# Optimization experiments

Hardware: AMD Instinct MI355X
Metric: run time of the kernel (lower is better)

Reference implementation:

```python
import jax, jax.numpy as jnp
import numpy as np

B, C, H, W = 4, 256, 64, 64
C8 = C // 8


def setup_inputs() -> dict:
    key = jax.random.key(0)
    ks = jax.random.split(key, 7)
    return {
        "x": jax.random.normal(ks[0], (B, C, H, W), dtype=jnp.float32),
        "Wq": jax.random.normal(ks[1], (C8, C), dtype=jnp.float32) * 0.05,
        "bq": jax.random.normal(ks[2], (C8,), dtype=jnp.float32) * 0.05,
        "Wk": jax.random.normal(ks[3], (C8, C), dtype=jnp.float32) * 0.05,
        "bk": jax.random.normal(ks[4], (C8,), dtype=jnp.float32) * 0.05,
        "Wv": jax.random.normal(ks[5], (C, C), dtype=jnp.float32) * 0.05,
        "bv": jax.random.normal(ks[6], (C,), dtype=jnp.float32) * 0.05,
        "gamma": jnp.zeros((1,), dtype=jnp.float32),
    }


def reference(x, Wq, bq, Wk, bk, Wv, bv, gamma):
    b, c, h, w = x.shape
    n = h * w
    xf = x.reshape(b, c, n)  # [B, C, N]
    # 1x1 convs == per-pixel linear maps over channels
    q = jnp.einsum('oc,bcn->bon', Wq, xf) + bq[None, :, None]  # [B, C/8, N]
    k = jnp.einsum('oc,bcn->bon', Wk, xf) + bk[None, :, None]  # [B, C/8, N]
    v = jnp.einsum('oc,bcn->bon', Wv, xf) + bv[None, :, None]  # [B, C, N]
    # s[b,i,j] = q_i . k_j ; torch softmax over dim=-2 (the i axis)
    s = jnp.einsum('bci,bcj->bij', q, k)  # [B, N, N]
    attn_T = jax.nn.softmax(s, axis=-2)
    # o[b,c,j] = sum_i v[b,c,i] * attn_T[b,i,j]
    o = jnp.einsum('bci,bij->bcj', v, attn_T)  # [B, C, N]
    return x + gamma[0] * o.reshape(b, c, h, w)
```

## Files before the change

kernel.cpp:

```cpp
#include <hip/hip_runtime.h>
#include <hip/hip_bf16.h>


typedef float  f32x16 __attribute__((ext_vector_type(16)));
typedef float  f32x4  __attribute__((ext_vector_type(4)));
typedef short  s16x8  __attribute__((ext_vector_type(8)));
typedef unsigned int u32;
typedef unsigned int u32x4 __attribute__((ext_vector_type(4)));

__device__ __forceinline__ s16x8 ld16(const ushort* p) {
  return *reinterpret_cast<const s16x8*>(p);
}
__device__ __forceinline__ ushort f2bf(float f) {
  return (ushort)((__float_as_uint(f) + 0x8000u) >> 16);
}
__device__ __forceinline__ u32 cvt_pk_bf16(float lo, float hi) {
  u32 r;
  asm("v_cvt_pk_bf16_f32 %0, %1, %2" : "=v"(r) : "v"(lo), "v"(hi));
  return r;
}

__global__ void wf_kernel(const float* __restrict__ Wq, const float* __restrict__ Wk,
                          const float* __restrict__ Wv,
                          const float* __restrict__ bq, const float* __restrict__ bk,
                          const float* __restrict__ bv, ushort* __restrict__ WF) {
  const int blk = blockIdx.x;
  const int ob = blk / 17, kb = blk % 17;
  const int t = threadIdx.x;
  const int l = t >> 3, e = t & 7;
  const int l31 = l & 31, g = l >> 5;
  const int o = ob * 32 + l31;
  float val;
  if (kb == 16) {
    float bias = (ob == 0) ? bq[l31] : (ob == 1) ? bk[l31] : bv[o - 64];
    val = (g == 0 && e == 0) ? bias : 0.f;
  } else {
    const int c = kb * 16 + (e & 3) + ((e >> 2) << 3) + (g << 2);
    val = (ob == 0) ? Wq[l31 * 256 + c]
        : (ob == 1) ? Wk[l31 * 256 + c]
                    : Wv[(o - 64) * 256 + c];
  }
  WF[((size_t)blk * 64 + l) * 8 + e] = f2bf(val);
}

__global__ __launch_bounds__(640) void proj_kernel(
    const float* __restrict__ x, const ushort* __restrict__ WF,
    ushort* __restrict__ qA, ushort* __restrict__ kB, ushort* __restrict__ vA) {
  __shared__ ushort xbf[17 * 1024];
  __shared__ ushort obuf[20480];
  const int bid = blockIdx.x;
  const int b = bid >> 6, w = bid & 63;
  const int n0 = w << 6;
  const int t = threadIdx.x;

  const float* xb = x + (size_t)(b * 256) * 4096 + n0;
  #pragma unroll
  for (int kk = 0; kk < 7; ++kk) {
    int idx = t + kk * 640;
    if (idx < 4096) {
      int c = idx >> 4, nq = idx & 15;
      f32x4 xv = *reinterpret_cast<const f32x4*>(xb + (size_t)c * 4096 + nq * 4);
      int kb = c >> 4, r = c & 15;
      int gg = (r >> 2) & 1, ee = (r & 3) + ((r >> 3) << 2);
      #pragma unroll
      for (int u = 0; u < 4; ++u) {
        int n = nq * 4 + u;
        xbf[kb * 1024 + ((n >> 5) * 2 + gg) * 256 + (n & 31) * 8 + ee] = f2bf(xv[u]);
      }
    }
  }
  for (int u = t; u < 1024; u += 640) {
    int gg = (u >> 8) & 1, ee = u & 7;
    xbf[16 * 1024 + u] = (gg == 0 && ee == 0) ? (ushort)0x3F80 : (ushort)0;
  }
  __syncthreads();

  const int l = t & 63;
  const int wv = __builtin_amdgcn_readfirstlane(t >> 6);
  const int l31 = l & 31, g = l >> 5;

  s16x8 wf[17];
  #pragma unroll
  for (int kb = 0; kb < 17; ++kb)
    wf[kb] = ld16(WF + ((size_t)(wv * 17 + kb) * 64 + l) * 8);

  f32x16 acc[2];
  #pragma unroll
  for (int nb = 0; nb < 2; ++nb)
    #pragma unroll
    for (int r = 0; r < 16; ++r) acc[nb][r] = 0.f;

  #pragma unroll
  for (int nb = 0; nb < 2; ++nb)
    #pragma unroll
    for (int kb = 0; kb < 17; ++kb)
      acc[nb] = __builtin_amdgcn_mfma_f32_32x32x16_bf16(
          wf[kb], ld16(xbf + kb * 1024 + (nb * 2 + g) * 256 + l31 * 8), acc[nb], 0, 0, 0);

  if (wv < 2) {
    const int obase = wv * 2048;
    #pragma unroll
    for (int nb = 0; nb < 2; ++nb)
      #pragma unroll
      for (int r = 0; r < 16; ++r)
        obuf[obase + (nb * 4 + (r >> 3) * 2 + g) * 256 + l31 * 8 + (r & 3) + (((r >> 2) & 1) << 2)]
            = f2bf(acc[nb][r]);
  } else {
    const int gv = (l31 >> 2) & 1;
    const int ev = (l31 & 3) + (((l31 >> 3) & 1) << 2);
    #pragma unroll
    for (int nb = 0; nb < 2; ++nb) {
      const int fi = (nb * 2 + (l31 >> 4)) * 2 + gv;
      #pragma unroll
      for (int r = 0; r < 16; ++r) {
        const int c = (wv - 2) * 32 + (r & 3) + ((r >> 2) << 3) + (g << 2);
        obuf[4096 + (fi * 256 + c) * 8 + ev] = f2bf(acc[nb][r]);
      }
    }
  }
  __syncthreads();

  const size_t qbase = (size_t)(b * 64 + w) * 2048;
  const size_t vbase = ((size_t)b * 512 + w * 8) * 2048;
  #pragma unroll
  for (int kk = 0; kk < 4; ++kk) {
    int ci = t + kk * 640;
    int off = ci * 8;
    s16x8 val = ld16(obuf + off);
    ushort* dst = (off < 2048) ? (qA + qbase + off)
                : (off < 4096) ? (kB + qbase + off - 2048)
                               : (vA + vbase + off - 4096);
    *reinterpret_cast<s16x8*>(dst) = val;
  }
}

__global__ __launch_bounds__(512, 2) void attn_kernel(
    const ushort* __restrict__ qA, const ushort* __restrict__ kB, const ushort* __restrict__ vA,
    const float* __restrict__ x, const float* __restrict__ gamma, float* __restrict__ out) {
  __shared__ ushort pls[2 * 4 * 2 * 2 * 64 * 8];
  __shared__ float lsr[8][64];
  const int bid = blockIdx.x;
  const int b = bid & 3;
  const int jt = bid >> 2;
  const int j0 = jt << 6;
  const int t = threadIdx.x;
  const int l = t & 63;
  const int wv = __builtin_amdgcn_readfirstlane(t >> 6);
  const int is = wv & 3, cs = wv >> 2;
  const int l31 = l & 31, g = l >> 5;
  const float gm = gamma[0];

  s16x8 kf[2];
  #pragma unroll
  for (int dh = 0; dh < 2; ++dh)
    kf[dh] = ld16(kB + (size_t)((b * 64 + jt) * 8 + cs * 4 + dh * 2 + g) * 256 + l31 * 8);

  f32x16 acc[2];
  #pragma unroll
  for (int jb = 0; jb < 2; ++jb)
    #pragma unroll
    for (int r = 0; r < 16; ++r) acc[jb][r] = 0.f;
  float lsum = 1e-30f;
  const int c0 = wv * 32 + l31;

  s16x8 qf0, qf1;
  {
    const int i_sub = is * 32;
    const size_t qb = (size_t)((b * 64 + (i_sub >> 6)) * 8 + ((i_sub >> 5) & 1) * 4 + g) * 256 + l31 * 8;
    qf0 = ld16(qA + qb);
    qf1 = ld16(qA + qb + 512);
  }

  for (int wi = 0; wi < 32; ++wi) {
    const int buf = wi & 1;
    s16x8 vf[8];
    #pragma unroll
    for (int m = 0; m < 8; ++m)
      vf[m] = ld16(vA + ((size_t)(b * 512 + (wi * 8 + m) * 2 + g) * 256 + c0) * 8);

    f32x16 s;
    #pragma unroll
    for (int r = 0; r < 16; ++r) s[r] = 0.f;
    s = __builtin_amdgcn_mfma_f32_32x32x16_bf16(qf0, kf[0], s, 0, 0, 0);
    s = __builtin_amdgcn_mfma_f32_32x32x16_bf16(qf1, kf[1], s, 0, 0, 0);
    if (wi < 31) {
      const int i_sub = (wi + 1) * 128 + is * 32;
      const size_t qb = (size_t)((b * 64 + (i_sub >> 6)) * 8 + ((i_sub >> 5) & 1) * 4 + g) * 256 + l31 * 8;
      qf0 = ld16(qA + qb);
      qf1 = ld16(qA + qb + 512);
    }
    float p[16], ls = 0.f;
    #pragma unroll
    for (int r = 0; r < 16; ++r) {
      p[r] = __builtin_amdgcn_exp2f(__builtin_fmaf(s[r], 1.4426950408889634f, -24.0f));
      ls += p[r];
    }
    lsum += ls;
    u32x4 w0, w1;
    #pragma unroll
    for (int q = 0; q < 4; ++q) {
      w0[q] = cvt_pk_bf16(p[2 * q],     p[2 * q + 1]);
      w1[q] = cvt_pk_bf16(p[8 + 2 * q], p[8 + 2 * q + 1]);
    }
    ushort* wp = pls + ((((buf * 4 + is) * 2 + cs) * 2 + 0) * 64 + l) * 8;
    *reinterpret_cast<s16x8*>(wp)       = __builtin_bit_cast(s16x8, w0);
    *reinterpret_cast<s16x8*>(wp + 512) = __builtin_bit_cast(s16x8, w1);
    __syncthreads();

    s16x8 pball[8][2];
    #pragma unroll
    for (int m = 0; m < 8; ++m)
      #pragma unroll
      for (int jb = 0; jb < 2; ++jb)
        pball[m][jb] = ld16(pls + ((((buf * 4 + (m >> 1)) * 2 + jb) * 2 + (m & 1)) * 64 + l) * 8);
    __builtin_amdgcn_s_setprio(1);
    #pragma unroll
    for (int m = 0; m < 8; ++m) {
      acc[0] = __builtin_amdgcn_mfma_f32_32x32x16_bf16(vf[m], pball[m][0], acc[0], 0, 0, 0);
      acc[1] = __builtin_amdgcn_mfma_f32_32x32x16_bf16(vf[m], pball[m][1], acc[1], 0, 0, 0);
    }
    __builtin_amdgcn_s_setprio(0);
  }

  lsr[wv][l] = lsum;
  __syncthreads();
  #pragma unroll
  for (int jb = 0; jb < 2; ++jb) {
    float tot = 0.f;
    #pragma unroll
    for (int i2 = 0; i2 < 4; ++i2)
      tot += lsr[jb * 4 + i2][l31] + lsr[jb * 4 + i2][l31 + 32];
    const float sc = gm / tot;
    #pragma unroll
    for (int r = 0; r < 16; ++r) {
      const int c = wv * 32 + (r & 3) + ((r >> 2) << 3) + (g << 2);
      const size_t idx = (size_t)(b * 256 + c) * 4096 + j0 + jb * 32 + l31;
      out[idx] = __builtin_fmaf(sc, acc[jb][r], x[idx]);
    }
  }
}

extern "C" void kernel_launch(void* const* d_in, const int* in_sizes, int n_in,
                              void* d_out, int out_size, void* d_ws, size_t ws_size,
                              hipStream_t stream) {
  const float* x     = (const float*)d_in[0];
  const float* Wq    = (const float*)d_in[1];
  const float* bq    = (const float*)d_in[2];
  const float* Wk    = (const float*)d_in[3];
  const float* bk    = (const float*)d_in[4];
  const float* Wv    = (const float*)d_in[5];
  const float* bv    = (const float*)d_in[6];
  const float* gamma = (const float*)d_in[7];
  float* out = (float*)d_out;

  char* ws = (char*)d_ws;
  ushort* WF = (ushort*)(ws);
  ushort* qA = (ushort*)(ws + 262144);
  ushort* kB = (ushort*)(ws + 262144 + 1048576);
  ushort* vA = (ushort*)(ws + 262144 + 2097152);

  wf_kernel  <<<170, 512, 0, stream>>>(Wq, Wk, Wv, bq, bk, bv, WF);
  proj_kernel<<<256, 640, 0, stream>>>(x, WF, qA, kB, vA);
  attn_kernel<<<256, 512, 0, stream>>>(qA, kB, vA, x, gamma, out);
}
```

Baseline: 75.15 us.

## Warp-specialize attention kernel into score producers and PV consumers with pipelined barriers

Splits the 8 waves of attn_kernel into 4 producer waves that compute QK scores, exponentiate and write bf16 probabilities to double-buffered LDS, and 4 consumer waves that load V and run the PV MFMAs one iteration behind. Consumer tiles grow to 64 channels by 64 columns so each P fragment feeds more MFMAs, and V loads are prefetched a step ahead. This aims to overlap the exp/score work with the PV matrix multiplies and cut redundant P reads. In exchange, producer and consumer waves are tied together by raw s_barrier, and the consumer waves hold more accumulator and V registers.

Result: faster. 63.97 us (-14.9%).

```diff
diff --git a/kernel.cpp b/kernel.cpp
--- a/kernel.cpp
+++ b/kernel.cpp
@@ -137,8 +137,8 @@
 __global__ __launch_bounds__(512, 2) void attn_kernel(
     const ushort* __restrict__ qA, const ushort* __restrict__ kB, const ushort* __restrict__ vA,
     const float* __restrict__ x, const float* __restrict__ gamma, float* __restrict__ out) {
-  __shared__ ushort pls[2 * 4 * 2 * 2 * 64 * 8];
-  __shared__ float lsr[8][64];
+  __shared__ ushort pls[2 * 8 * 2 * 512];
+  __shared__ float lsr[4][2][64];
   const int bid = blockIdx.x;
   const int b = bid & 3;
   const int jt = bid >> 2;
@@ -146,96 +146,130 @@
   const int t = threadIdx.x;
   const int l = t & 63;
   const int wv = __builtin_amdgcn_readfirstlane(t >> 6);
-  const int is = wv & 3, cs = wv >> 2;
   const int l31 = l & 31, g = l >> 5;
   const float gm = gamma[0];
 
-  s16x8 kf[2];
-  #pragma unroll
-  for (int dh = 0; dh < 2; ++dh)
-    kf[dh] = ld16(kB + (size_t)((b * 64 + jt) * 8 + cs * 4 + dh * 2 + g) * 256 + l31 * 8);
-
-  f32x16 acc[2];
-  #pragma unroll
-  for (int jb = 0; jb < 2; ++jb)
-    #pragma unroll
-    for (int r = 0; r < 16; ++r) acc[jb][r] = 0.f;
-  float lsum = 1e-30f;
-  const int c0 = wv * 32 + l31;
-
-  s16x8 qf0, qf1;
-  {
-    const int i_sub = is * 32;
-    const size_t qb = (size_t)((b * 64 + (i_sub >> 6)) * 8 + ((i_sub >> 5) & 1) * 4 + g) * 256 + l31 * 8;
-    qf0 = ld16(qA + qb);
-    qf1 = ld16(qA + qb + 512);
-  }
-
-  for (int wi = 0; wi < 32; ++wi) {
-    const int buf = wi & 1;
-    s16x8 vf[8];
-    #pragma unroll
-    for (int m = 0; m < 8; ++m)
-      vf[m] = ld16(vA + ((size_t)(b * 512 + (wi * 8 + m) * 2 + g) * 256 + c0) * 8);
-
-    f32x16 s;
-    #pragma unroll
-    for (int r = 0; r < 16; ++r) s[r] = 0.f;
-    s = __builtin_amdgcn_mfma_f32_32x32x16_bf16(qf0, kf[0], s, 0, 0, 0);
-    s = __builtin_amdgcn_mfma_f32_32x32x16_bf16(qf1, kf[1], s, 0, 0, 0);
-    if (wi < 31) {
-      const int i_sub = (wi + 1) * 128 + is * 32;
-      const size_t qb = (size_t)((b * 64 + (i_sub >> 6)) * 8 + ((i_sub >> 5) & 1) * 4 + g) * 256 + l31 * 8;
+  if (wv >= 4) {
+    const int sw = wv - 4;
+    s16x8 kf00, kf01, kf10, kf11;
+    {
+      const size_t kb0 = (size_t)((b * 64 + jt) * 8 + g) * 256 + l31 * 8;
+      kf00 = ld16(kB + kb0);
+      kf01 = ld16(kB + kb0 + 512);
+      kf10 = ld16(kB + kb0 + 1024);
+      kf11 = ld16(kB + kb0 + 1536);
+    }
+    float lsum0 = 1e-30f, lsum1 = 1e-30f;
+    s16x8 qf0, qf1;
+    {
+      const size_t qb = (size_t)((b * 64 + (sw >> 1)) * 8 + (sw & 1) * 4 + g) * 256 + l31 * 8;
       qf0 = ld16(qA + qb);
       qf1 = ld16(qA + qb + 512);
     }
-    float p[16], ls = 0.f;
-    #pragma unroll
-    for (int r = 0; r < 16; ++r) {
-      p[r] = __builtin_amdgcn_exp2f(__builtin_fmaf(s[r], 1.4426950408889634f, -24.0f));
-      ls += p[r];
-    }
-    lsum += ls;
-    u32x4 w0, w1;
-    #pragma unroll
-    for (int q = 0; q < 4; ++q) {
-      w0[q] = cvt_pk_bf16(p[2 * q],     p[2 * q + 1]);
-      w1[q] = cvt_pk_bf16(p[8 + 2 * q], p[8 + 2 * q + 1]);
-    }
-    ushort* wp = pls + ((((buf * 4 + is) * 2 + cs) * 2 + 0) * 64 + l) * 8;
-    *reinterpret_cast<s16x8*>(wp)       = __builtin_bit_cast(s16x8, w0);
-    *reinterpret_cast<s16x8*>(wp + 512) = __builtin_bit_cast(s16x8, w1);
-    __syncthreads();
-
-    s16x8 pball[8][2];
-    #pragma unroll
-    for (int m = 0; m < 8; ++m)
+    for (int reg = 0; reg <= 32; ++reg) {
+      if (reg < 32) {
+        const int wi = reg, buf = wi & 1;
+        f32x16 s0, s1;
+        #pragma unroll
+        for (int r = 0; r < 16; ++r) { s0[r] = 0.f; s1[r] = 0.f; }
+        s0 = __builtin_amdgcn_mfma_f32_32x32x16_bf16(qf0, kf00, s0, 0, 0, 0);
+        s0 = __builtin_amdgcn_mfma_f32_32x32x16_bf16(qf1, kf01, s0, 0, 0, 0);
+        s1 = __builtin_amdgcn_mfma_f32_32x32x16_bf16(qf0, kf10, s1, 0, 0, 0);
+        s1 = __builtin_amdgcn_mfma_f32_32x32x16_bf16(qf1, kf11, s1, 0, 0, 0);
+        if (wi < 31) {
+          const size_t qb = (size_t)((b * 64 + (wi + 1) * 2 + (sw >> 1)) * 8 + (sw & 1) * 4 + g) * 256 + l31 * 8;
+          qf0 = ld16(qA + qb);
+          qf1 = ld16(qA + qb + 512);
+        }
+        float p0[16], p1[16], ls0 = 0.f, ls1 = 0.f;
+        #pragma unroll
+        for (int r = 0; r < 16; ++r) {
+          p0[r] = __builtin_amdgcn_exp2f(__builtin_fmaf(s0[r], 1.4426950408889634f, -24.0f));
+          p1[r] = __builtin_amdgcn_exp2f(__builtin_fmaf(s1[r], 1.4426950408889634f, -24.0f));
+          ls0 += p0[r];
+          ls1 += p1[r];
+        }
+        lsum0 += ls0;
+        lsum1 += ls1;
+        u32x4 w00, w01, w10, w11;
+        #pragma unroll
+        for (int q = 0; q < 4; ++q) {
+          w00[q] = cvt_pk_bf16(p0[2 * q],     p0[2 * q + 1]);
+          w01[q] = cvt_pk_bf16(p0[8 + 2 * q], p0[8 + 2 * q + 1]);
+          w10[q] = cvt_pk_bf16(p1[2 * q],     p1[2 * q + 1]);
+          w11[q] = cvt_pk_bf16(p1[8 + 2 * q], p1[8 + 2 * q + 1]);
+        }
+        ushort* p00 = pls + ((buf * 16 + (2 * sw + 0) * 2 + 0) * 512) + l * 8;
+        ushort* p01 = pls + ((buf * 16 + (2 * sw + 1) * 2 + 0) * 512) + l * 8;
+        ushort* p10 = pls + ((buf * 16 + (2 * sw + 0) * 2 + 1) * 512) + l * 8;
+        ushort* p11 = pls + ((buf * 16 + (2 * sw + 1) * 2 + 1) * 512) + l * 8;
+        *reinterpret_cast<s16x8*>(p00) = __builtin_bit_cast(s16x8, w00);
+        *reinterpret_cast<s16x8*>(p01) = __builtin_bit_cast(s16x8, w01);
+        *reinterpret_cast<s16x8*>(p10) = __builtin_bit_cast(s16x8, w10);
+        *reinterpret_cast<s16x8*>(p11) = __builtin_bit_cast(s16x8, w11);
+      } else {
+        lsr[sw][0][l] = lsum0;
+        lsr[sw][1][l] = lsum1;
+      }
+      asm volatile("s_waitcnt lgkmcnt(0)" ::: "memory");
+      __builtin_amdgcn_s_barrier();
+      __builtin_amdgcn_sched_barrier(0);
+    }
+  } else {
+    const int pv = wv;
+    const ushort* vbase = vA + ((size_t)(b * 512 + g) * 256 + pv * 64 + l31) * 8;
+    f32x16 acc[2][2];
+    #pragma unroll
+    for (int cg = 0; cg < 2; ++cg)
       #pragma unroll
       for (int jb = 0; jb < 2; ++jb)
-        pball[m][jb] = ld16(pls + ((((buf * 4 + (m >> 1)) * 2 + jb) * 2 + (m & 1)) * 64 + l) * 8);
-    __builtin_amdgcn_s_setprio(1);
-    #pragma unroll
-    for (int m = 0; m < 8; ++m) {
-      acc[0] = __builtin_amdgcn_mfma_f32_32x32x16_bf16(vf[m], pball[m][0], acc[0], 0, 0, 0);
-      acc[1] = __builtin_amdgcn_mfma_f32_32x32x16_bf16(vf[m], pball[m][1], acc[1], 0, 0, 0);
-    }
-    __builtin_amdgcn_s_setprio(0);
-  }
-
-  lsr[wv][l] = lsum;
-  __syncthreads();
-  #pragma unroll
-  for (int jb = 0; jb < 2; ++jb) {
-    float tot = 0.f;
-    #pragma unroll
-    for (int i2 = 0; i2 < 4; ++i2)
-      tot += lsr[jb * 4 + i2][l31] + lsr[jb * 4 + i2][l31 + 32];
-    const float sc = gm / tot;
-    #pragma unroll
-    for (int r = 0; r < 16; ++r) {
-      const int c = wv * 32 + (r & 3) + ((r >> 2) << 3) + (g << 2);
-      const size_t idx = (size_t)(b * 256 + c) * 4096 + j0 + jb * 32 + l31;
-      out[idx] = __builtin_fmaf(sc, acc[jb][r], x[idx]);
+        #pragma unroll
+        for (int r = 0; r < 16; ++r) acc[cg][jb][r] = 0.f;
+    s16x8 vf[8][2];
+    for (int reg = 0; reg <= 32; ++reg) {
+      if (reg == 0) {
+        #pragma unroll
+        for (int m = 0; m < 8; ++m) {
+          vf[m][0] = ld16(vbase + (size_t)m * 4096);
+          vf[m][1] = ld16(vbase + (size_t)m * 4096 + 256);
+        }
+      } else {
+        const int wi = reg - 1, buf = wi & 1;
+        __builtin_amdgcn_s_setprio(1);
+        #pragma unroll
+        for (int m = 0; m < 8; ++m) {
+          s16x8 pf0 = ld16(pls + ((buf * 16 + m * 2 + 0) * 512) + l * 8);
+          s16x8 pf1 = ld16(pls + ((buf * 16 + m * 2 + 1) * 512) + l * 8);
+          acc[0][0] = __builtin_amdgcn_mfma_f32_32x32x16_bf16(vf[m][0], pf0, acc[0][0], 0, 0, 0);
+          acc[1][0] = __builtin_amdgcn_mfma_f32_32x32x16_bf16(vf[m][1], pf0, acc[1][0], 0, 0, 0);
+          acc[0][1] = __builtin_amdgcn_mfma_f32_32x32x16_bf16(vf[m][0], pf1, acc[0][1], 0, 0, 0);
+          acc[1][1] = __builtin_amdgcn_mfma_f32_32x32x16_bf16(vf[m][1], pf1, acc[1][1], 0, 0, 0);
+          if (reg < 32) {
+            vf[m][0] = ld16(vbase + (size_t)(reg * 8 + m) * 4096);
+            vf[m][1] = ld16(vbase + (size_t)(reg * 8 + m) * 4096 + 256);
+          }
+        }
+        __builtin_amdgcn_s_setprio(0);
+      }
+      __builtin_amdgcn_s_barrier();
+      __builtin_amdgcn_sched_barrier(0);
+    }
+    #pragma unroll
+    for (int jb = 0; jb < 2; ++jb) {
+      float tot = 0.f;
+      #pragma unroll
+      for (int sw2 = 0; sw2 < 4; ++sw2)
+        tot += lsr[sw2][jb][l31] + lsr[sw2][jb][l31 + 32];
+      const float sc = gm / tot;
+      #pragma unroll
+      for (int cg = 0; cg < 2; ++cg) {
+        #pragma unroll
+        for (int r = 0; r < 16; ++r) {
+          const int c = pv * 64 + cg * 32 + (r & 3) + ((r >> 2) << 3) + (g << 2);
+          const size_t idx = (size_t)(b * 256 + c) * 4096 + j0 + jb * 32 + l31;
+          out[idx] = __builtin_fmaf(sc, acc[cg][jb][r], x[idx]);
+        }
+      }
     }
   }
 }
```

## Warp-specialize attention into score/softmax producers and PV consumers

Applied to the files above, without the earlier changes.

Splits the 8 waves of the attention block into 4 producer waves, which compute QK scores and exp and write P to LDS, and 4 consumer waves, which do the PV MFMAs. The two groups run one tile apart through a double-buffered LDS P buffer. Each block now covers 128 output columns and half the channels (grid indexing changed), so S is computed twice per column tile, once per channel half. The goal is to overlap softmax/exp work with the PV matmul and widen the column tile to reuse V loads. In exchange it duplicates QK work and uses a larger LDS footprint.

Result: slower. 84.46 us (+12.4%).

```diff
diff --git a/kernel.cpp b/kernel.cpp
--- a/kernel.cpp
+++ b/kernel.cpp
@@ -137,105 +137,129 @@
 __global__ __launch_bounds__(512, 2) void attn_kernel(
     const ushort* __restrict__ qA, const ushort* __restrict__ kB, const ushort* __restrict__ vA,
     const float* __restrict__ x, const float* __restrict__ gamma, float* __restrict__ out) {
-  __shared__ ushort pls[2 * 4 * 2 * 2 * 64 * 8];
-  __shared__ float lsr[8][64];
+  __shared__ ushort pls[2 * 8 * 4 * 512];
+  __shared__ float  lsr[4][4][64];
   const int bid = blockIdx.x;
-  const int b = bid & 3;
-  const int jt = bid >> 2;
-  const int j0 = jt << 6;
+  const int ch = bid & 1;
+  const int b  = (bid >> 1) & 3;
+  const int jt = bid >> 3;
+  const int j0 = jt << 7;
   const int t = threadIdx.x;
   const int l = t & 63;
   const int wv = __builtin_amdgcn_readfirstlane(t >> 6);
-  const int is = wv & 3, cs = wv >> 2;
   const int l31 = l & 31, g = l >> 5;
   const float gm = gamma[0];
 
-  s16x8 kf[2];
-  #pragma unroll
-  for (int dh = 0; dh < 2; ++dh)
-    kf[dh] = ld16(kB + (size_t)((b * 64 + jt) * 8 + cs * 4 + dh * 2 + g) * 256 + l31 * 8);
-
-  f32x16 acc[2];
-  #pragma unroll
-  for (int jb = 0; jb < 2; ++jb)
-    #pragma unroll
-    for (int r = 0; r < 16; ++r) acc[jb][r] = 0.f;
-  float lsum = 1e-30f;
-  const int c0 = wv * 32 + l31;
-
-  s16x8 qf0, qf1;
-  {
-    const int i_sub = is * 32;
-    const size_t qb = (size_t)((b * 64 + (i_sub >> 6)) * 8 + ((i_sub >> 5) & 1) * 4 + g) * 256 + l31 * 8;
-    qf0 = ld16(qA + qb);
-    qf1 = ld16(qA + qb + 512);
-  }
-
-  for (int wi = 0; wi < 32; ++wi) {
-    const int buf = wi & 1;
-    s16x8 vf[8];
-    #pragma unroll
-    for (int m = 0; m < 8; ++m)
-      vf[m] = ld16(vA + ((size_t)(b * 512 + (wi * 8 + m) * 2 + g) * 256 + c0) * 8);
-
-    f32x16 s;
-    #pragma unroll
-    for (int r = 0; r < 16; ++r) s[r] = 0.f;
-    s = __builtin_amdgcn_mfma_f32_32x32x16_bf16(qf0, kf[0], s, 0, 0, 0);
-    s = __builtin_amdgcn_mfma_f32_32x32x16_bf16(qf1, kf[1], s, 0, 0, 0);
-    if (wi < 31) {
-      const int i_sub = (wi + 1) * 128 + is * 32;
-      const size_t qb = (size_t)((b * 64 + (i_sub >> 6)) * 8 + ((i_sub >> 5) & 1) * 4 + g) * 256 + l31 * 8;
+  if (wv >= 4) {
+    const int sw = wv - 4;
+    s16x8 kf[4][2];
+    #pragma unroll
+    for (int jb = 0; jb < 4; ++jb)
+      #pragma unroll
+      for (int dh = 0; dh < 2; ++dh)
+        kf[jb][dh] = ld16(kB + (size_t)((b * 64 + jt * 2 + (jb >> 1)) * 8 + (jb & 1) * 4 + dh * 2 + g) * 256 + l31 * 8);
+    float lsum[4] = {1e-30f, 1e-30f, 1e-30f, 1e-30f};
+    s16x8 qf0, qf1;
+    {
+      const size_t qb = (size_t)((b * 64 + (sw >> 1)) * 8 + (sw & 1) * 4 + g) * 256 + l31 * 8;
       qf0 = ld16(qA + qb);
       qf1 = ld16(qA + qb + 512);
     }
-    float p[16], ls = 0.f;
-    #pragma unroll
-    for (int r = 0; r < 16; ++r) {
-      p[r] = __builtin_amdgcn_exp2f(__builtin_fmaf(s[r], 1.4426950408889634f, -24.0f));
-      ls += p[r];
-    }
-    lsum += ls;
-    u32x4 w0, w1;
-    #pragma unroll
-    for (int q = 0; q < 4; ++q) {
-      w0[q] = cvt_pk_bf16(p[2 * q],     p[2 * q + 1]);
-      w1[q] = cvt_pk_bf16(p[8 + 2 * q], p[8 + 2 * q + 1]);
-    }
-    ushort* wp = pls + ((((buf * 4 + is) * 2 + cs) * 2 + 0) * 64 + l) * 8;
-    *reinterpret_cast<s16x8*>(wp)       = __builtin_bit_cast(s16x8, w0);
-    *reinterpret_cast<s16x8*>(wp + 512) = __builtin_bit_cast(s16x8, w1);
-    __syncthreads();
-
-    s16x8 pball[8][2];
-    #pragma unroll
-    for (int m = 0; m < 8; ++m)
-      #pragma unroll
-      for (int jb = 0; jb < 2; ++jb)
-        pball[m][jb] = ld16(pls + ((((buf * 4 + (m >> 1)) * 2 + jb) * 2 + (m & 1)) * 64 + l) * 8);
-    __builtin_amdgcn_s_setprio(1);
-    #pragma unroll
-    for (int m = 0; m < 8; ++m) {
-      acc[0] = __builtin_amdgcn_mfma_f32_32x32x16_bf16(vf[m], pball[m][0], acc[0], 0, 0, 0);
-      acc[1] = __builtin_amdgcn_mfma_f32_32x32x16_bf16(vf[m], pball[m][1], acc[1], 0, 0, 0);
-    }
-    __builtin_amdgcn_s_setprio(0);
-  }
-
-  lsr[wv][l] = lsum;
-  __syncthreads();
-  #pragma unroll
-  for (int jb = 0; jb < 2; ++jb) {
-    float tot = 0.f;
-    #pragma unroll
-    for (int i2 = 0; i2 < 4; ++i2)
-      tot += lsr[jb * 4 + i2][l31] + lsr[jb * 4 + i2][l31 + 32];
-    const float sc = gm / tot;
-    #pragma unroll
-    for (int r = 0; r < 16; ++r) {
-      const int c = wv * 32 + (r & 3) + ((r >> 2) << 3) + (g << 2);
-      const size_t idx = (size_t)(b * 256 + c) * 4096 + j0 + jb * 32 + l31;
-      out[idx] = __builtin_fmaf(sc, acc[jb][r], x[idx]);
+    for (int reg = 0; reg <= 32; ++reg) {
+      if (reg < 32) {
+        const int wi = reg, buf = wi & 1;
+        f32x16 s[4];
+        #pragma unroll
+        for (int jb = 0; jb < 4; ++jb)
+          #pragma unroll
+          for (int r = 0; r < 16; ++r) s[jb][r] = 0.f;
+        __builtin_amdgcn_s_setprio(1);
+        #pragma unroll
+        for (int jb = 0; jb < 4; ++jb) {
+          s[jb] = __builtin_amdgcn_mfma_f32_32x32x16_bf16(qf0, kf[jb][0], s[jb], 0, 0, 0);
+          s[jb] = __builtin_amdgcn_mfma_f32_32x32x16_bf16(qf1, kf[jb][1], s[jb], 0, 0, 0);
+        }
+        __builtin_amdgcn_s_setprio(0);
+        if (wi < 31) {
+          const size_t qb = (size_t)((b * 64 + (wi + 1) * 2 + (sw >> 1)) * 8 + (sw & 1) * 4 + g) * 256 + l31 * 8;
+          qf0 = ld16(qA + qb);
+          qf1 = ld16(qA + qb + 512);
+        }
+        #pragma unroll
+        for (int jb = 0; jb < 4; ++jb) {
+          float p[16], ls = 0.f;
+          #pragma unroll
+          for (int r = 0; r < 16; ++r) {
+            p[r] = __builtin_amdgcn_exp2f(__builtin_fmaf(s[jb][r], 1.4426950408889634f, -24.0f));
+            ls += p[r];
+          }
+          lsum[jb] += ls;
+          u32x4 wlo, whi;
+          #pragma unroll
+          for (int q = 0; q < 4; ++q) {
+            wlo[q] = cvt_pk_bf16(p[2 * q],     p[2 * q + 1]);
+            whi[q] = cvt_pk_bf16(p[8 + 2 * q], p[8 + 2 * q + 1]);
+          }
+          ushort* plo = pls + ((buf * 8 + 2 * sw + 0) * 4 + jb) * 512 + l * 8;
+          ushort* phi = pls + ((buf * 8 + 2 * sw + 1) * 4 + jb) * 512 + l * 8;
+          *reinterpret_cast<s16x8*>(plo) = __builtin_bit_cast(s16x8, wlo);
+          *reinterpret_cast<s16x8*>(phi) = __builtin_bit_cast(s16x8, whi);
+        }
+      } else {
+        #pragma unroll
+        for (int jb = 0; jb < 4; ++jb) lsr[sw][jb][l] = lsum[jb];
+      }
+      asm volatile("s_waitcnt lgkmcnt(0)" ::: "memory");
+      __builtin_amdgcn_s_barrier();
+      __builtin_amdgcn_sched_barrier(0);
+    }
+  } else {
+    const int pv = wv;
+    const int c0 = ch * 128 + pv * 32 + l31;
+    const ushort* vbase = vA + ((size_t)(b * 512 + g) * 256 + c0) * 8;
+    f32x16 acc[4];
+    #pragma unroll
+    for (int jb = 0; jb < 4; ++jb)
+      #pragma unroll
+      for (int r = 0; r < 16; ++r) acc[jb][r] = 0.f;
+    s16x8 vf[8];
+    for (int reg = 0; reg <= 32; ++reg) {
+      if (reg == 0) {
+        #pragma unroll
+        for (int m = 0; m < 8; ++m)
+          vf[m] = ld16(vbase + (size_t)m * 4096);
+      } else {
+        const int wi = reg - 1, buf = wi & 1;
+        #pragma unroll
+        for (int m = 0; m < 8; ++m) {
+          s16x8 pf0 = ld16(pls + ((buf * 8 + m) * 4 + 0) * 512 + l * 8);
+          s16x8 pf1 = ld16(pls + ((buf * 8 + m) * 4 + 1) * 512 + l * 8);
+          s16x8 pf2 = ld16(pls + ((buf * 8 + m) * 4 + 2) * 512 + l * 8);
+          s16x8 pf3 = ld16(pls + ((buf * 8 + m) * 4 + 3) * 512 + l * 8);
+          acc[0] = __builtin_amdgcn_mfma_f32_32x32x16_bf16(vf[m], pf0, acc[0], 0, 0, 0);
+          acc[1] = __builtin_amdgcn_mfma_f32_32x32x16_bf16(vf[m], pf1, acc[1], 0, 0, 0);
+          acc[2] = __builtin_amdgcn_mfma_f32_32x32x16_bf16(vf[m], pf2, acc[2], 0, 0, 0);
+          acc[3] = __builtin_amdgcn_mfma_f32_32x32x16_bf16(vf[m], pf3, acc[3], 0, 0, 0);
+          if (reg < 32)
+            vf[m] = ld16(vbase + (size_t)(reg * 8 + m) * 4096);
+        }
+      }
+      __builtin_amdgcn_s_barrier();
+      __builtin_amdgcn_sched_barrier(0);
+    }
+    #pragma unroll
+    for (int jb = 0; jb < 4; ++jb) {
+      float tot = 0.f;
+      #pragma unroll
+      for (int sw2 = 0; sw2 < 4; ++sw2)
+        tot += lsr[sw2][jb][l31] + lsr[sw2][jb][l31 + 32];
+      const float sc = gm / tot;
+      #pragma unroll
+      for (int r = 0; r < 16; ++r) {
+        const int c = ch * 128 + pv * 32 + (r & 3) + ((r >> 2) << 3) + (g << 2);
+        const size_t idx = (size_t)(b * 256 + c) * 4096 + j0 + jb * 32 + l31;
+        out[idx] = __builtin_fmaf(sc, acc[jb][r], x[idx]);
+      }
     }
   }
 }
```

## Split attention work so each wave owns a column slice and skips LDS exchange

Applied to the files above, without the earlier changes.

The attention kernel now gives each wave a 32-column query slice, half of the key range and 128 output channels. Each wave feeds its softmax probabilities straight from registers into the PV MFMAs. This removes the per-iteration LDS write, the __syncthreads and the LDS reload of probabilities that the old split needed. The cost is that QK scores and exponentials are computed twice, once per channel half. The two key halves are also combined once at the end through shared memory.

Result: slower. 77.12 us (+2.6%).

```diff
diff --git a/kernel.cpp b/kernel.cpp
--- a/kernel.cpp
+++ b/kernel.cpp
@@ -137,55 +137,59 @@
 __global__ __launch_bounds__(512, 2) void attn_kernel(
     const ushort* __restrict__ qA, const ushort* __restrict__ kB, const ushort* __restrict__ vA,
     const float* __restrict__ x, const float* __restrict__ gamma, float* __restrict__ out) {
-  __shared__ ushort pls[2 * 4 * 2 * 2 * 64 * 8];
-  __shared__ float lsr[8][64];
+  __shared__ float sacc[4 * 4 * 16 * 64];
+  __shared__ float lsr[4][64];
   const int bid = blockIdx.x;
-  const int b = bid & 3;
-  const int jt = bid >> 2;
-  const int j0 = jt << 6;
+  const int chalf = bid & 1;
+  const int b = (bid >> 1) & 3;
+  const int jgroup = bid >> 3;
   const int t = threadIdx.x;
   const int l = t & 63;
   const int wv = __builtin_amdgcn_readfirstlane(t >> 6);
-  const int is = wv & 3, cs = wv >> 2;
+  const int js = wv >> 1, ih = wv & 1;
   const int l31 = l & 31, g = l >> 5;
+  const int j0 = (jgroup * 4 + js) * 32;
   const float gm = gamma[0];
 
-  s16x8 kf[2];
-  #pragma unroll
-  for (int dh = 0; dh < 2; ++dh)
-    kf[dh] = ld16(kB + (size_t)((b * 64 + jt) * 8 + cs * 4 + dh * 2 + g) * 256 + l31 * 8);
-
-  f32x16 acc[2];
-  #pragma unroll
-  for (int jb = 0; jb < 2; ++jb)
-    #pragma unroll
-    for (int r = 0; r < 16; ++r) acc[jb][r] = 0.f;
-  float lsum = 1e-30f;
-  const int c0 = wv * 32 + l31;
-
+  s16x8 kf0, kf1;
+  {
+    const size_t kb0 = (size_t)((b * 64 + (j0 >> 6)) * 8 + ((j0 >> 5) & 1) * 4 + g) * 256 + l31 * 8;
+    kf0 = ld16(kB + kb0);
+    kf1 = ld16(kB + kb0 + 512);
+  }
+  const int i_base = ih * 2048;
   s16x8 qf0, qf1;
   {
-    const int i_sub = is * 32;
-    const size_t qb = (size_t)((b * 64 + (i_sub >> 6)) * 8 + ((i_sub >> 5) & 1) * 4 + g) * 256 + l31 * 8;
+    const size_t qb = (size_t)((b * 64 + (i_base >> 6)) * 8 + (((i_base >> 5) & 1)) * 4 + g) * 256 + l31 * 8;
     qf0 = ld16(qA + qb);
     qf1 = ld16(qA + qb + 512);
   }
-
-  for (int wi = 0; wi < 32; ++wi) {
-    const int buf = wi & 1;
-    s16x8 vf[8];
-    #pragma unroll
-    for (int m = 0; m < 8; ++m)
-      vf[m] = ld16(vA + ((size_t)(b * 512 + (wi * 8 + m) * 2 + g) * 256 + c0) * 8);
-
+  const int c0 = chalf * 128 + l31;
+  s16x8 vf[4][2];
+  #pragma unroll
+  for (int cg = 0; cg < 4; ++cg) {
+    const size_t va = ((size_t)(b * 512 + (ih * 128) * 2 + g) * 256 + c0 + cg * 32) * 8;
+    vf[cg][0] = ld16(vA + va);
+    vf[cg][1] = ld16(vA + va + 4096);
+  }
+
+  f32x16 acc[4];
+  #pragma unroll
+  for (int cg = 0; cg < 4; ++cg)
+    #pragma unroll
+    for (int r = 0; r < 16; ++r) acc[cg][r] = 0.f;
+  float lsum = 1e-30f;
+
+  for (int wi = 0; wi < 64; ++wi) {
+    const int i0 = i_base + wi * 32;
     f32x16 s;
     #pragma unroll
     for (int r = 0; r < 16; ++r) s[r] = 0.f;
-    s = __builtin_amdgcn_mfma_f32_32x32x16_bf16(qf0, kf[0], s, 0, 0, 0);
-    s = __builtin_amdgcn_mfma_f32_32x32x16_bf16(qf1, kf[1], s, 0, 0, 0);
-    if (wi < 31) {
-      const int i_sub = (wi + 1) * 128 + is * 32;
-      const size_t qb = (size_t)((b * 64 + (i_sub >> 6)) * 8 + ((i_sub >> 5) & 1) * 4 + g) * 256 + l31 * 8;
+    s = __builtin_amdgcn_mfma_f32_32x32x16_bf16(qf0, kf0, s, 0, 0, 0);
+    s = __builtin_amdgcn_mfma_f32_32x32x16_bf16(qf1, kf1, s, 0, 0, 0);
+    if (wi < 63) {
+      const int in = i0 + 32;
+      const size_t qb = (size_t)((b * 64 + (in >> 6)) * 8 + ((in >> 5) & 1) * 4 + g) * 256 + l31 * 8;
       qf0 = ld16(qA + qb);
       qf1 = ld16(qA + qb + 512);
     }
@@ -202,40 +206,42 @@
       w0[q] = cvt_pk_bf16(p[2 * q],     p[2 * q + 1]);
       w1[q] = cvt_pk_bf16(p[8 + 2 * q], p[8 + 2 * q + 1]);
     }
-    ushort* wp = pls + ((((buf * 4 + is) * 2 + cs) * 2 + 0) * 64 + l) * 8;
-    *reinterpret_cast<s16x8*>(wp)       = __builtin_bit_cast(s16x8, w0);
-    *reinterpret_cast<s16x8*>(wp + 512) = __builtin_bit_cast(s16x8, w1);
-    __syncthreads();
-
-    s16x8 pball[8][2];
-    #pragma unroll
-    for (int m = 0; m < 8; ++m)
-      #pragma unroll
-      for (int jb = 0; jb < 2; ++jb)
-        pball[m][jb] = ld16(pls + ((((buf * 4 + (m >> 1)) * 2 + jb) * 2 + (m & 1)) * 64 + l) * 8);
-    __builtin_amdgcn_s_setprio(1);
-    #pragma unroll
-    for (int m = 0; m < 8; ++m) {
-      acc[0] = __builtin_amdgcn_mfma_f32_32x32x16_bf16(vf[m], pball[m][0], acc[0], 0, 0, 0);
-      acc[1] = __builtin_amdgcn_mfma_f32_32x32x16_bf16(vf[m], pball[m][1], acc[1], 0, 0, 0);
-    }
-    __builtin_amdgcn_s_setprio(0);
-  }
-
-  lsr[wv][l] = lsum;
+    const s16x8 pb0 = __builtin_bit_cast(s16x8, w0);
+    const s16x8 pb1 = __builtin_bit_cast(s16x8, w1);
+    #pragma unroll
+    for (int cg = 0; cg < 4; ++cg) {
+      acc[cg] = __builtin_amdgcn_mfma_f32_32x32x16_bf16(vf[cg][0], pb0, acc[cg], 0, 0, 0);
+      acc[cg] = __builtin_amdgcn_mfma_f32_32x32x16_bf16(vf[cg][1], pb1, acc[cg], 0, 0, 0);
+      if (wi < 63) {
+        const size_t va = ((size_t)(b * 512 + (ih * 128 + wi * 2 + 2) * 2 + g) * 256 + c0 + cg * 32) * 8;
+        vf[cg][0] = ld16(vA + va);
+        vf[cg][1] = ld16(vA + va + 4096);
+      }
+    }
+  }
+
+  float lsum_f = lsum + __shfl_xor(lsum, 32, 64);
+  if (ih == 1) {
+    #pragma unroll
+    for (int cg = 0; cg < 4; ++cg)
+      #pragma unroll
+      for (int r = 0; r < 16; ++r)
+        sacc[((js * 4 + cg) * 16 + r) * 64 + l] = acc[cg][r];
+    lsr[js][l] = lsum_f;
+  }
   __syncthreads();
-  #pragma unroll
-  for (int jb = 0; jb < 2; ++jb) {
-    float tot = 0.f;
-    #pragma unroll
-    for (int i2 = 0; i2 < 4; ++i2)
-      tot += lsr[jb * 4 + i2][l31] + lsr[jb * 4 + i2][l31 + 32];
+  if (ih == 0) {
+    const float tot = lsum_f + lsr[js][l];
     const float sc = gm / tot;
     #pragma unroll
-    for (int r = 0; r < 16; ++r) {
-      const int c = wv * 32 + (r & 3) + ((r >> 2) << 3) + (g << 2);
-      const size_t idx = (size_t)(b * 256 + c) * 4096 + j0 + jb * 32 + l31;
-      out[idx] = __builtin_fmaf(sc, acc[jb][r], x[idx]);
+    for (int cg = 0; cg < 4; ++cg) {
+      #pragma unroll
+      for (int r = 0; r < 16; ++r) {
+        const float o = acc[cg][r] + sacc[((js * 4 + cg) * 16 + r) * 64 + l];
+        const int c = chalf * 128 + cg * 32 + (r & 3) + ((r >> 2) << 3) + (g << 2);
+        const size_t idx = (size_t)(b * 256 + c) * 4096 + j0 + l31;
+        out[idx] = __builtin_fmaf(sc, o, x[idx]);
+      }
     }
   }
 }
```
